# Kernel optimization log

Measured on AMD Instinct MI355X. Metric: run time of the kernel, lower is better.

The kernel has to match this reference:

```python
import jax, jax.numpy as jnp
import numpy as np

WS = 7          # window size
HEADS = 8
SHIFT = WS // 2  # shift=True -> 3
C = 256
KD = C // HEADS  # key_dim = 32
LN_EPS = 1e-3    # keras LayerNormalization default


def setup_inputs() -> dict:
    key = jax.random.key(0)
    ks = jax.random.split(key, 12)
    s = 1.0 / np.sqrt(C)
    x = jax.random.normal(ks[0], (16, 112, 112, C), dtype=jnp.float32)
    wq = jax.random.normal(ks[1], (C, HEADS, KD), dtype=jnp.float32) * s
    bq = jnp.zeros((HEADS, KD), dtype=jnp.float32)
    wk = jax.random.normal(ks[2], (C, HEADS, KD), dtype=jnp.float32) * s
    bk = jnp.zeros((HEADS, KD), dtype=jnp.float32)
    wv = jax.random.normal(ks[3], (C, HEADS, KD), dtype=jnp.float32) * s
    bv = jnp.zeros((HEADS, KD), dtype=jnp.float32)
    wo = jax.random.normal(ks[4], (HEADS, KD, C), dtype=jnp.float32) * s
    bo = jnp.zeros((C,), dtype=jnp.float32)
    gamma = jnp.ones((C,), dtype=jnp.float32)
    beta = jnp.zeros((C,), dtype=jnp.float32)
    return {"x": x, "wq": wq, "bq": bq, "wk": wk, "bk": bk,
            "wv": wv, "bv": bv, "wo": wo, "bo": bo,
            "gamma": gamma, "beta": beta}


def _swin_window_attn(x, wq, bq, wk, bk, wv, bv, wo, bo, gamma, beta):
    b, h, w, c = x.shape
    pad_h = (WS - h % WS) % WS
    pad_w = (WS - w % WS) % WS
    if pad_h or pad_w:
        x = jnp.pad(x, ((0, 0), (0, pad_h), (0, pad_w), (0, 0)))
    hp, wp = h + pad_h, w + pad_w
    if SHIFT > 0:
        x = jnp.roll(x, shift=(-SHIFT, -SHIFT), axis=(1, 2))
    nh, nw = hp // WS, wp // WS
    # window partition: (b, nh, WS, nw, WS, c) -> (b*nh*nw, WS*WS, c)
    win = x.reshape(b, nh, WS, nw, WS, c).transpose(0, 1, 3, 2, 4, 5)
    win = win.reshape(b * nh * nw, WS * WS, c)
    # multi-head attention (keras MHA: query scaled by 1/sqrt(key_dim))
    q = jnp.einsum("nsc,chd->nshd", win, wq) + bq
    k = jnp.einsum("nsc,chd->nshd", win, wk) + bk
    v = jnp.einsum("nsc,chd->nshd", win, wv) + bv
    scores = jnp.einsum("nqhd,nkhd->nhqk", q, k) / jnp.sqrt(jnp.float32(KD)).astype(q.dtype)
    probs = jax.nn.softmax(scores, axis=-1)
    ctx = jnp.einsum("nhqk,nkhd->nqhd", probs, v)
    attn = jnp.einsum("nqhd,hdc->nqc", ctx, wo) + bo
    # residual + LayerNorm
    y = attn + win
    mu = jnp.mean(y, axis=-1, keepdims=True)
    var = jnp.mean(jnp.square(y - mu), axis=-1, keepdims=True)
    y = (y - mu) * jax.lax.rsqrt(var + LN_EPS) * gamma + beta
    # window reverse
    out = y.reshape(b, nh, nw, WS, WS, c).transpose(0, 1, 3, 2, 4, 5)
    out = out.reshape(b, hp, wp, c)
    if SHIFT > 0:
        out = jnp.roll(out, shift=(SHIFT, SHIFT), axis=(1, 2))
    if pad_h or pad_w:
        out = out[:, :h, :w, :]
    return out


def reference(x, wq, bq, wk, bk, wv, bv, wo, bo, gamma, beta):
    return _swin_window_attn(x, wq, bq, wk, bk, wv, bv, wo, bo, gamma, beta)
```

## Files before the change

### kernel.cpp

```cpp
#include <hip/hip_runtime.h>
#include <hip/hip_bf16.h>

typedef __attribute__((ext_vector_type(8))) short short8;
typedef __attribute__((ext_vector_type(4))) short short4v;
typedef __attribute__((ext_vector_type(4))) float float4v;
typedef __attribute__((ext_vector_type(2))) unsigned int uint2v;

#define LDS_BYTES 144384
#define XBF_OFF   0
#define VT_OFF    33792
#define Q_OFF     70656
#define K_OFF     104448
#define P_OFF     70656
#define CTX_OFF   33792
#define Y_OFF     70656


__device__ __forceinline__ unsigned short f2bf_rn(float f) {
    union { __hip_bfloat16 b; unsigned short u; } v;
    v.b = __float2bfloat16(f);
    return v.u;
}
__device__ __forceinline__ unsigned int pk2bf(float a, float b) {
    union { __hip_bfloat162 h; unsigned int u; } v;
    v.h = __float22bfloat162_rn(make_float2(a, b));
    return v.u;
}
__device__ __forceinline__ float bf2f(unsigned short h) {
    union { unsigned int u; float f; } v; v.u = ((unsigned int)h) << 16;
    return v.f;
}

__global__ void prep_weights(const float* __restrict__ wq, const float* __restrict__ wk,
                             const float* __restrict__ wv, const float* __restrict__ wo,
                             unsigned short* __restrict__ wfrag) {
    int tid = blockIdx.x * 256 + threadIdx.x;
    if (tid >= 4 * 65536) return;
    int m = tid >> 16;
    int e = tid & 65535;
    int j = e & 7;
    int lane = (e >> 3) & 63;
    int nt2 = (e >> 9) & 15;
    int ks = e >> 13;
    int c = ks * 32 + (lane >> 4) * 8 + j;
    int o = nt2 * 16 + (lane & 15);
    const float* W = (m == 0) ? wq : (m == 1) ? wk : (m == 2) ? wv : wo;
    wfrag[tid] = f2bf_rn(W[c * 256 + o]);
}

__global__ __launch_bounds__(1024, 4) void swin_fused(
    const float* __restrict__ x,
    const unsigned short* __restrict__ wfrag,
    const float* __restrict__ bq, const float* __restrict__ bk,
    const float* __restrict__ bv, const float* __restrict__ bo,
    const float* __restrict__ gamma, const float* __restrict__ beta,
    float* __restrict__ out)
{
    extern __shared__ char smem[];
    const int tid = threadIdx.x;
    const int w    = tid >> 6;
    const int h    = w & 7;
    const int half = w >> 3;
    const int l   = tid & 63;
    const int l15 = l & 15;
    const int l4  = l >> 4;
    const int nt2 = 2 * h + half;

    const int sxA = (l15 & 8) << 2;
    const int sxS = (l4  & 2) << 4;

    const int blk = blockIdx.x;
    const int bb  = blk >> 8;
    const int wh  = (blk >> 4) & 15;
    const int ww  = blk & 15;

    char* XbfC = smem + XBF_OFF;

    for (int idx = tid; idx < 64 * 64; idx += 1024) {
        const int tok = idx >> 6;
        const int c4  = idx & 63;
        float4v f = (float4v){0.f, 0.f, 0.f, 0.f};
        if (tok < 49) {
            const int i = tok / 7;
            const int j = tok - 7 * i;
            int gr = wh * 7 + i + 3; if (gr >= 112) gr -= 112;
            int gc = ww * 7 + j + 3; if (gc >= 112) gc -= 112;
            f = *(const float4v*)(x + (((size_t)bb * 112 + gr) * 112 + gc) * 256 + c4 * 4);
        }
        uint2v u;
        u.x = pk2bf(f.x, f.y);
        u.y = pk2bf(f.z, f.w);
        *(uint2v*)(XbfC + ((tok * 528 + c4 * 8) ^ ((tok & 8) << 2))) = u;
    }
    __syncthreads();

    char* QsC = smem + Q_OFF;
    char* KsC = smem + K_OFF;
    unsigned short* Vt = (unsigned short*)(smem + VT_OFF);

    const float* biases[3] = { bq, bk, bv };
#pragma unroll
    for (int m = 0; m < 3; ++m) {
        float4v acc[4];
#pragma unroll
        for (int mt = 0; mt < 4; ++mt) acc[mt] = (float4v){0.f, 0.f, 0.f, 0.f};
        const unsigned short* wmat = wfrag + m * 65536;
        __builtin_amdgcn_s_setprio(1);
#pragma unroll
        for (int ks = 0; ks < 8; ++ks) {
            short8 bfr = *(const short8*)(wmat + ((ks * 16 + nt2) * 64 + l) * 8);
#pragma unroll
            for (int mt = 0; mt < 4; ++mt) {
                short8 afr = *(const short8*)(XbfC + (((mt * 16 + l15) * 528 + (ks * 32 + l4 * 8) * 2) ^ sxA));
                acc[mt] = __builtin_amdgcn_mfma_f32_16x16x32_bf16(afr, bfr, acc[mt], 0, 0, 0);
            }
        }
        __builtin_amdgcn_s_setprio(0);
        const int o = nt2 * 16 + l15;
        const float bias = biases[m][o];
        if (m == 2) {
            const int d = half * 16 + l15;
#pragma unroll
            for (int mt = 0; mt < 4; ++mt) {
                uint2v u;
                u.x = pk2bf(acc[mt][0] + bias, acc[mt][1] + bias);
                u.y = pk2bf(acc[mt][2] + bias, acc[mt][3] + bias);
                *(uint2v*)(Vt + h * 2304 + d * 72 + mt * 16 + l4 * 4) = u;
            }
        } else {
            char* dst = (m == 0) ? QsC : KsC;
#pragma unroll
            for (int mt = 0; mt < 4; ++mt) {
                const int tok0 = mt * 16 + l4 * 4;
#pragma unroll
                for (int r = 0; r < 4; ++r)
                    *(unsigned short*)(dst + (((tok0 + r) * 528 + o * 2) ^ sxS)) = f2bf_rn(acc[mt][r] + bias);
            }
        }
    }
    __syncthreads();

    float4v sa[4][2];
#pragma unroll
    for (int mt = 0; mt < 4; ++mt)
#pragma unroll
        for (int nt = 0; nt < 2; ++nt)
            sa[mt][nt] = (float4v){0.f, 0.f, 0.f, 0.f};
    {
        short8 kfr[4], qfr[2];
#pragma unroll
        for (int mt = 0; mt < 4; ++mt)
            kfr[mt] = *(const short8*)(KsC + (((mt * 16 + l15) * 528 + (32 * h + l4 * 8) * 2) ^ sxA));
#pragma unroll
        for (int nt = 0; nt < 2; ++nt)
            qfr[nt] = *(const short8*)(QsC + (((32 * half + nt * 16 + l15) * 528 + (32 * h + l4 * 8) * 2) ^ sxA));
        __builtin_amdgcn_s_setprio(1);
#pragma unroll
        for (int mt = 0; mt < 4; ++mt)
#pragma unroll
            for (int nt = 0; nt < 2; ++nt)
                sa[mt][nt] = __builtin_amdgcn_mfma_f32_16x16x32_bf16(kfr[mt], qfr[nt], sa[mt][nt], 0, 0, 0);
        __builtin_amdgcn_s_setprio(0);
    }
    __syncthreads();

    unsigned short* Ph = (unsigned short*)(smem + P_OFF) + h * 4608;
    const float SCALE = 0.17677669529663687f;
#pragma unroll
    for (int nt = 0; nt < 2; ++nt) {
        float sv[4][4];
        float mx = -1e30f;
#pragma unroll
        for (int mt = 0; mt < 4; ++mt)
#pragma unroll
            for (int r = 0; r < 4; ++r) {
                const bool valid = (mt < 3) || ((l4 == 0) && (r == 0));
                sv[mt][r] = valid ? sa[mt][nt][r] * SCALE : -1e30f;
                mx = fmaxf(mx, sv[mt][r]);
            }
        mx = fmaxf(mx, __shfl_xor(mx, 16, 64));
        mx = fmaxf(mx, __shfl_xor(mx, 32, 64));
        float p[4][4];
        float sum = 0.f;
#pragma unroll
        for (int mt = 0; mt < 4; ++mt)
#pragma unroll
            for (int r = 0; r < 4; ++r) {
                p[mt][r] = __expf(sv[mt][r] - mx);
                sum += p[mt][r];
            }
        sum += __shfl_xor(sum, 16, 64);
        sum += __shfl_xor(sum, 32, 64);
        const float inv = 1.f / sum;
        const int q = 32 * half + nt * 16 + l15;
#pragma unroll
        for (int mt = 0; mt < 4; ++mt) {
            uint2v u;
            u.x = pk2bf(p[mt][0] * inv, p[mt][1] * inv);
            u.y = pk2bf(p[mt][2] * inv, p[mt][3] * inv);
            *(uint2v*)(Ph + q * 72 + mt * 16 + l4 * 4) = u;
        }
    }

    float4v ca[2][2];
#pragma unroll
    for (int mtl = 0; mtl < 2; ++mtl)
#pragma unroll
        for (int nt = 0; nt < 2; ++nt)
            ca[mtl][nt] = (float4v){0.f, 0.f, 0.f, 0.f};
#pragma unroll
    for (int ks = 0; ks < 2; ++ks) {
        short8 afr[2];
#pragma unroll
        for (int mtl = 0; mtl < 2; ++mtl)
            afr[mtl] = *(const short8*)(Ph + (32 * half + mtl * 16 + l15) * 72 + ks * 32 + l4 * 8);
        __builtin_amdgcn_s_setprio(1);
#pragma unroll
        for (int nt = 0; nt < 2; ++nt) {
            short8 bfr = *(const short8*)(Vt + h * 2304 + (nt * 16 + l15) * 72 + ks * 32 + l4 * 8);
#pragma unroll
            for (int mtl = 0; mtl < 2; ++mtl)
                ca[mtl][nt] = __builtin_amdgcn_mfma_f32_16x16x32_bf16(afr[mtl], bfr, ca[mtl][nt], 0, 0, 0);
        }
        __builtin_amdgcn_s_setprio(0);
    }
    __syncthreads();

    char* CtxC = smem + CTX_OFF;
#pragma unroll
    for (int nt = 0; nt < 2; ++nt) {
        const int o = 32 * h + nt * 16 + l15;
#pragma unroll
        for (int mtl = 0; mtl < 2; ++mtl) {
            const int tok0 = (2 * half + mtl) * 16 + l4 * 4;
#pragma unroll
            for (int r = 0; r < 4; ++r)
                *(unsigned short*)(CtxC + (((tok0 + r) * 528 + o * 2) ^ sxS)) = f2bf_rn(ca[mtl][nt][r]);
        }
    }
    __syncthreads();

    float4v oa[4];
#pragma unroll
    for (int mt = 0; mt < 4; ++mt) oa[mt] = (float4v){0.f, 0.f, 0.f, 0.f};
    const unsigned short* womat = wfrag + 3 * 65536;
    __builtin_amdgcn_s_setprio(1);
#pragma unroll
    for (int ks = 0; ks < 8; ++ks) {
        short8 bfr = *(const short8*)(womat + ((ks * 16 + nt2) * 64 + l) * 8);
#pragma unroll
        for (int mt = 0; mt < 4; ++mt) {
            short8 afr = *(const short8*)(CtxC + (((mt * 16 + l15) * 528 + (ks * 32 + l4 * 8) * 2) ^ sxA));
            oa[mt] = __builtin_amdgcn_mfma_f32_16x16x32_bf16(afr, bfr, oa[mt], 0, 0, 0);
        }
    }
    __builtin_amdgcn_s_setprio(0);
    float* Y = (float*)(smem + Y_OFF);
    {
        const int cout = nt2 * 16 + l15;
        const float bias = bo[cout];
#pragma unroll
        for (int mt = 0; mt < 4; ++mt)
#pragma unroll
            for (int r = 0; r < 4; ++r) {
                const int tok = mt * 16 + l4 * 4 + r;
                const float xv = bf2f(*(const unsigned short*)(XbfC + ((tok * 528 + cout * 2) ^ sxS)));
                Y[tok * 260 + cout] = oa[mt][r] + bias + xv;
            }
    }
    __syncthreads();

    const float4v g4  = *(const float4v*)(gamma + l * 4);
    const float4v be4 = *(const float4v*)(beta + l * 4);
#pragma unroll
    for (int t = 0; t < 4; ++t) {
        const int tok = w + t * 16;
        if (tok < 49) {
            float4v f = *(const float4v*)(Y + tok * 260 + l * 4);
            float sum = f.x + f.y + f.z + f.w;
            float sq  = f.x * f.x + f.y * f.y + f.z * f.z + f.w * f.w;
#pragma unroll
            for (int msk = 1; msk < 64; msk <<= 1) {
                sum += __shfl_xor(sum, msk, 64);
                sq  += __shfl_xor(sq,  msk, 64);
            }
            const float mu   = sum * (1.f / 256.f);
            const float var  = sq * (1.f / 256.f) - mu * mu;
            const float rstd = rsqrtf(var + 1e-3f);
            const int i = tok / 7;
            const int j = tok - 7 * i;
            int gr = wh * 7 + i + 3; if (gr >= 112) gr -= 112;
            int gc = ww * 7 + j + 3; if (gc >= 112) gc -= 112;
            float4v o4;
            o4.x = (f.x - mu) * rstd * g4.x + be4.x;
            o4.y = (f.y - mu) * rstd * g4.y + be4.y;
            o4.z = (f.z - mu) * rstd * g4.z + be4.z;
            o4.w = (f.w - mu) * rstd * g4.w + be4.w;
            *(float4v*)(out + (((size_t)bb * 112 + gr) * 112 + gc) * 256 + l * 4) = o4;
        }
    }
}

extern "C" void kernel_launch(void* const* d_in, const int* in_sizes, int n_in,
                              void* d_out, int out_size, void* d_ws, size_t ws_size,
                              hipStream_t stream) {
    const float* x     = (const float*)d_in[0];
    const float* wq    = (const float*)d_in[1];
    const float* bq    = (const float*)d_in[2];
    const float* wk    = (const float*)d_in[3];
    const float* bk    = (const float*)d_in[4];
    const float* wv    = (const float*)d_in[5];
    const float* bv    = (const float*)d_in[6];
    const float* wo    = (const float*)d_in[7];
    const float* bo    = (const float*)d_in[8];
    const float* gamma = (const float*)d_in[9];
    const float* beta  = (const float*)d_in[10];
    float* out = (float*)d_out;
    unsigned short* wfrag = (unsigned short*)d_ws;

    prep_weights<<<1024, 256, 0, stream>>>(wq, wk, wv, wo, wfrag);

    hipFuncSetAttribute((const void*)swin_fused,
                        hipFuncAttributeMaxDynamicSharedMemorySize, LDS_BYTES);
    swin_fused<<<4096, 1024, LDS_BYTES, stream>>>(x, wfrag, bq, bk, bv, bo, gamma, beta, out);
}
```

Before: 301.0 us.

## Fuse Q/K/V projections into one pass and drop LDS XOR swizzle

Merges the three separate Q, K, V projection loops into a single k-loop, so each X fragment is read from LDS once and feeds three MFMAs instead of being reloaded per projection. Removes the XOR swizzle on the LDS layout and relies on the 264-element padded row stride alone to avoid bank conflicts. Moves the residual add of the bf16 input from the per-fragment Y write into the vectorized LayerNorm load. This raises register pressure from three accumulator sets and may bring back LDS bank conflicts that the swizzle was preventing.

```diff
diff --git a/kernel.cpp b/kernel.cpp
--- a/kernel.cpp
+++ b/kernel.cpp
@@ -14,7 +14,6 @@
 #define P_OFF     70656
 #define CTX_OFF   33792
 #define Y_OFF     70656
-
 
 __device__ __forceinline__ unsigned short f2bf_rn(float f) {
     union { __hip_bfloat16 b; unsigned short u; } v;
@@ -66,15 +65,12 @@
     const int l4  = l >> 4;
     const int nt2 = 2 * h + half;
 
-    const int sxA = (l15 & 8) << 2;
-    const int sxS = (l4  & 2) << 4;
-
     const int blk = blockIdx.x;
     const int bb  = blk >> 8;
     const int wh  = (blk >> 4) & 15;
     const int ww  = blk & 15;
 
-    char* XbfC = smem + XBF_OFF;
+    unsigned short* Xbf = (unsigned short*)(smem + XBF_OFF);
 
     for (int idx = tid; idx < 64 * 64; idx += 1024) {
         const int tok = idx >> 6;
@@ -90,52 +86,67 @@
         uint2v u;
         u.x = pk2bf(f.x, f.y);
         u.y = pk2bf(f.z, f.w);
-        *(uint2v*)(XbfC + ((tok * 528 + c4 * 8) ^ ((tok & 8) << 2))) = u;
-    }
-    __syncthreads();
-
-    char* QsC = smem + Q_OFF;
-    char* KsC = smem + K_OFF;
+        *(uint2v*)(Xbf + tok * 264 + c4 * 4) = u;
+    }
+    __syncthreads();
+
+    unsigned short* Qs = (unsigned short*)(smem + Q_OFF);
+    unsigned short* Ks = (unsigned short*)(smem + K_OFF);
     unsigned short* Vt = (unsigned short*)(smem + VT_OFF);
 
-    const float* biases[3] = { bq, bk, bv };
-#pragma unroll
-    for (int m = 0; m < 3; ++m) {
-        float4v acc[4];
-#pragma unroll
-        for (int mt = 0; mt < 4; ++mt) acc[mt] = (float4v){0.f, 0.f, 0.f, 0.f};
-        const unsigned short* wmat = wfrag + m * 65536;
-        __builtin_amdgcn_s_setprio(1);
+    {
+        float4v accQ[4], accK[4], accV[4];
+#pragma unroll
+        for (int mt = 0; mt < 4; ++mt) {
+            accQ[mt] = (float4v){0.f, 0.f, 0.f, 0.f};
+            accK[mt] = (float4v){0.f, 0.f, 0.f, 0.f};
+            accV[mt] = (float4v){0.f, 0.f, 0.f, 0.f};
+        }
+        const unsigned short* wqf = wfrag;
+        const unsigned short* wkf = wfrag + 65536;
+        const unsigned short* wvf = wfrag + 2 * 65536;
 #pragma unroll
         for (int ks = 0; ks < 8; ++ks) {
-            short8 bfr = *(const short8*)(wmat + ((ks * 16 + nt2) * 64 + l) * 8);
-#pragma unroll
-            for (int mt = 0; mt < 4; ++mt) {
-                short8 afr = *(const short8*)(XbfC + (((mt * 16 + l15) * 528 + (ks * 32 + l4 * 8) * 2) ^ sxA));
-                acc[mt] = __builtin_amdgcn_mfma_f32_16x16x32_bf16(afr, bfr, acc[mt], 0, 0, 0);
-            }
-        }
-        __builtin_amdgcn_s_setprio(0);
+            const int woff = ((ks * 16 + nt2) * 64 + l) * 8;
+            short8 bq_ = *(const short8*)(wqf + woff);
+            short8 bk_ = *(const short8*)(wkf + woff);
+            short8 bv_ = *(const short8*)(wvf + woff);
+            short8 afr[4];
+#pragma unroll
+            for (int mt = 0; mt < 4; ++mt)
+                afr[mt] = *(const short8*)(Xbf + (mt * 16 + l15) * 264 + ks * 32 + l4 * 8);
+            __builtin_amdgcn_s_setprio(1);
+#pragma unroll
+            for (int mt = 0; mt < 4; ++mt)
+                accQ[mt] = __builtin_amdgcn_mfma_f32_16x16x32_bf16(afr[mt], bq_, accQ[mt], 0, 0, 0);
+#pragma unroll
+            for (int mt = 0; mt < 4; ++mt)
+                accK[mt] = __builtin_amdgcn_mfma_f32_16x16x32_bf16(afr[mt], bk_, accK[mt], 0, 0, 0);
+#pragma unroll
+            for (int mt = 0; mt < 4; ++mt)
+                accV[mt] = __builtin_amdgcn_mfma_f32_16x16x32_bf16(afr[mt], bv_, accV[mt], 0, 0, 0);
+            __builtin_amdgcn_s_setprio(0);
+        }
         const int o = nt2 * 16 + l15;
-        const float bias = biases[m][o];
-        if (m == 2) {
-            const int d = half * 16 + l15;
-#pragma unroll
-            for (int mt = 0; mt < 4; ++mt) {
-                uint2v u;
-                u.x = pk2bf(acc[mt][0] + bias, acc[mt][1] + bias);
-                u.y = pk2bf(acc[mt][2] + bias, acc[mt][3] + bias);
-                *(uint2v*)(Vt + h * 2304 + d * 72 + mt * 16 + l4 * 4) = u;
-            }
-        } else {
-            char* dst = (m == 0) ? QsC : KsC;
-#pragma unroll
-            for (int mt = 0; mt < 4; ++mt) {
-                const int tok0 = mt * 16 + l4 * 4;
-#pragma unroll
-                for (int r = 0; r < 4; ++r)
-                    *(unsigned short*)(dst + (((tok0 + r) * 528 + o * 2) ^ sxS)) = f2bf_rn(acc[mt][r] + bias);
-            }
+        const float biasq = bq[o];
+        const float biask = bk[o];
+        const float biasv = bv[o];
+#pragma unroll
+        for (int mt = 0; mt < 4; ++mt) {
+            const int tok0 = mt * 16 + l4 * 4;
+#pragma unroll
+            for (int r = 0; r < 4; ++r) {
+                Qs[(tok0 + r) * 264 + o] = f2bf_rn(accQ[mt][r] + biasq);
+                Ks[(tok0 + r) * 264 + o] = f2bf_rn(accK[mt][r] + biask);
+            }
+        }
+        const int d = half * 16 + l15;
+#pragma unroll
+        for (int mt = 0; mt < 4; ++mt) {
+            uint2v u;
+            u.x = pk2bf(accV[mt][0] + biasv, accV[mt][1] + biasv);
+            u.y = pk2bf(accV[mt][2] + biasv, accV[mt][3] + biasv);
+            *(uint2v*)(Vt + h * 2304 + d * 72 + mt * 16 + l4 * 4) = u;
         }
     }
     __syncthreads();
@@ -150,10 +161,10 @@
         short8 kfr[4], qfr[2];
 #pragma unroll
         for (int mt = 0; mt < 4; ++mt)
-            kfr[mt] = *(const short8*)(KsC + (((mt * 16 + l15) * 528 + (32 * h + l4 * 8) * 2) ^ sxA));
+            kfr[mt] = *(const short8*)(Ks + (mt * 16 + l15) * 264 + 32 * h + l4 * 8);
 #pragma unroll
         for (int nt = 0; nt < 2; ++nt)
-            qfr[nt] = *(const short8*)(QsC + (((32 * half + nt * 16 + l15) * 528 + (32 * h + l4 * 8) * 2) ^ sxA));
+            qfr[nt] = *(const short8*)(Qs + (32 * half + nt * 16 + l15) * 264 + 32 * h + l4 * 8);
         __builtin_amdgcn_s_setprio(1);
 #pragma unroll
         for (int mt = 0; mt < 4; ++mt)
@@ -226,16 +237,17 @@
     }
     __syncthreads();
 
-    char* CtxC = smem + CTX_OFF;
+    unsigned short* Ctx = (unsigned short*)(smem + CTX_OFF);
 #pragma unroll
     for (int nt = 0; nt < 2; ++nt) {
         const int o = 32 * h + nt * 16 + l15;
 #pragma unroll
         for (int mtl = 0; mtl < 2; ++mtl) {
             const int tok0 = (2 * half + mtl) * 16 + l4 * 4;
-#pragma unroll
-            for (int r = 0; r < 4; ++r)
-                *(unsigned short*)(CtxC + (((tok0 + r) * 528 + o * 2) ^ sxS)) = f2bf_rn(ca[mtl][nt][r]);
+            Ctx[(tok0 + 0) * 264 + o] = f2bf_rn(ca[mtl][nt][0]);
+            Ctx[(tok0 + 1) * 264 + o] = f2bf_rn(ca[mtl][nt][1]);
+            Ctx[(tok0 + 2) * 264 + o] = f2bf_rn(ca[mtl][nt][2]);
+            Ctx[(tok0 + 3) * 264 + o] = f2bf_rn(ca[mtl][nt][3]);
         }
     }
     __syncthreads();
@@ -244,17 +256,19 @@
 #pragma unroll
     for (int mt = 0; mt < 4; ++mt) oa[mt] = (float4v){0.f, 0.f, 0.f, 0.f};
     const unsigned short* womat = wfrag + 3 * 65536;
-    __builtin_amdgcn_s_setprio(1);
 #pragma unroll
     for (int ks = 0; ks < 8; ++ks) {
         short8 bfr = *(const short8*)(womat + ((ks * 16 + nt2) * 64 + l) * 8);
-#pragma unroll
-        for (int mt = 0; mt < 4; ++mt) {
-            short8 afr = *(const short8*)(CtxC + (((mt * 16 + l15) * 528 + (ks * 32 + l4 * 8) * 2) ^ sxA));
-            oa[mt] = __builtin_amdgcn_mfma_f32_16x16x32_bf16(afr, bfr, oa[mt], 0, 0, 0);
-        }
-    }
-    __builtin_amdgcn_s_setprio(0);
+        short8 afr[4];
+#pragma unroll
+        for (int mt = 0; mt < 4; ++mt)
+            afr[mt] = *(const short8*)(Ctx + (mt * 16 + l15) * 264 + ks * 32 + l4 * 8);
+        __builtin_amdgcn_s_setprio(1);
+#pragma unroll
+        for (int mt = 0; mt < 4; ++mt)
+            oa[mt] = __builtin_amdgcn_mfma_f32_16x16x32_bf16(afr[mt], bfr, oa[mt], 0, 0, 0);
+        __builtin_amdgcn_s_setprio(0);
+    }
     float* Y = (float*)(smem + Y_OFF);
     {
         const int cout = nt2 * 16 + l15;
@@ -264,8 +278,7 @@
 #pragma unroll
             for (int r = 0; r < 4; ++r) {
                 const int tok = mt * 16 + l4 * 4 + r;
-                const float xv = bf2f(*(const unsigned short*)(XbfC + ((tok * 528 + cout * 2) ^ sxS)));
-                Y[tok * 260 + cout] = oa[mt][r] + bias + xv;
+                Y[tok * 260 + cout] = oa[mt][r] + bias;
             }
     }
     __syncthreads();
@@ -277,6 +290,11 @@
         const int tok = w + t * 16;
         if (tok < 49) {
             float4v f = *(const float4v*)(Y + tok * 260 + l * 4);
+            short4v xr = *(const short4v*)(Xbf + tok * 264 + l * 4);
+            f.x += bf2f((unsigned short)xr.x);
+            f.y += bf2f((unsigned short)xr.y);
+            f.z += bf2f((unsigned short)xr.z);
+            f.w += bf2f((unsigned short)xr.w);
             float sum = f.x + f.y + f.z + f.w;
             float sq  = f.x * f.x + f.y * f.y + f.z * f.z + f.w * f.w;
 #pragma unroll
```

New measurement: 277.6 us. -7.8%, faster.
